# Optimization experiments

Measured on AMD Instinct MI355X. Metric: run time of the kernel, lower is better.

The kernel has to match this reference:

```python
import jax, jax.numpy as jnp
import numpy as np

B, N, D, L = 64, 512, 256, 4


def setup_inputs() -> dict:
    key = jax.random.key(0)
    ks = jax.random.split(key, 10)
    scale = 1.0 / np.sqrt(D)
    x = jax.random.normal(ks[0], (B, N, D), dtype=jnp.float32)
    adj = (jax.random.uniform(ks[1], (B, N, N)) < 0.1).astype(jnp.float32)
    return {
        "x": x,
        "adj": adj,
        "w_attn_w": jax.random.normal(ks[2], (L, D, D), dtype=jnp.float32) * scale,
        "w_attn_b": jnp.zeros((L, D), dtype=jnp.float32),
        "lin0_w": jax.random.normal(ks[3], (L, D, D), dtype=jnp.float32) * scale,
        "lin0_b": jnp.zeros((L, D), dtype=jnp.float32),
        "lin1_w": jax.random.normal(ks[4], (L, D, D), dtype=jnp.float32) * scale,
        "lin1_b": jnp.zeros((L, D), dtype=jnp.float32),
        "final_w": jax.random.normal(ks[5], (D, D), dtype=jnp.float32) * scale,
        "final_b": jnp.zeros((D,), dtype=jnp.float32),
    }


def reference(x, adj, w_attn_w, w_attn_b, lin0_w, lin0_b, lin1_w, lin1_b, final_w, final_b):
    # set self-loops on the adjacency diagonal (in-place in the torch code)
    idx = jnp.arange(N)
    adj = adj.at[:, idx, idx].set(1.0)
    eye = 1e-5 * jnp.eye(N, dtype=x.dtype)
    attls = []
    for l in range(L):
        x0 = x
        # q = w_attn[l](x): torch Linear is x @ W.T + b, W: [out,in]
        q = jnp.einsum('bnd,od->bno', x, w_attn_w[l]) + w_attn_b[l]
        adj_attn = jax.nn.sigmoid(jnp.einsum('bij,bkj->bik', q, x))  # [B,N,N]
        adj_attn = (adj_attn + eye) * adj
        adj_attn = adj_attn / jnp.sum(adj_attn, axis=-1, keepdims=True)
        attls.append(adj_attn)
        x = jnp.einsum('bij,bjd->bid', adj_attn, x)
        x = jax.nn.relu(jnp.einsum('bnd,od->bno', x, lin0_w[l]) + lin0_b[l])
        x = jax.nn.relu(jnp.einsum('bnd,od->bno', x, lin1_w[l]) + lin1_b[l])
        x = x + x0
    x = jnp.einsum('bnd,od->bno', x, final_w) + final_b
    return (x, jnp.stack(attls))
```

## Files before the change

kernel.cpp:

```cpp
#include <hip/hip_runtime.h>
#include <cstdint>

#define B_ 64
#define N_ 512
#define D_ 256
#define L_ 4

typedef __bf16 bf16;
typedef __attribute__((ext_vector_type(8))) __bf16 bf16x8;
typedef __attribute__((ext_vector_type(4))) __bf16 bf16x4;
typedef __attribute__((ext_vector_type(4))) float f32x4;

#define MFMA16(a, b, c) __builtin_amdgcn_mfma_f32_16x16x32_bf16((a), (b), (c), 0, 0, 0)

__device__ __forceinline__ float sigmoidf_(float z) {
  return 1.0f / (1.0f + __expf(-z));
}


#define BARSYNC() do { \
    asm volatile("s_waitcnt lgkmcnt(0)\n\ts_barrier" ::: "memory"); \
    __builtin_amdgcn_sched_barrier(0); \
  } while (0)

#define UIDX(u) (((size_t)(u)) * 64 + lane)

__global__ __launch_bounds__(256) void pack_w(
    const float* __restrict__ src, bf16* __restrict__ dst)
{
  const int tid = threadIdx.x, lane = tid & 63;
  const int U = blockIdx.x * 4 + (tid >> 6);
  const int m = U >> 7, u = U & 127;
  const int r16 = u >> 3, kc = u & 7;
  const int row = r16 * 16 + (lane & 15);
  const int k0 = kc * 32 + (lane >> 4) * 8;
  const float* s = src + (size_t)m * D_ * D_ + (size_t)row * D_ + k0;
  const float4 v0 = *(const float4*)s;
  const float4 v1 = *(const float4*)(s + 4);
  bf16x8 o;
  o[0] = (bf16)v0.x; o[1] = (bf16)v0.y; o[2] = (bf16)v0.z; o[3] = (bf16)v0.w;
  o[4] = (bf16)v1.x; o[5] = (bf16)v1.y; o[6] = (bf16)v1.z; o[7] = (bf16)v1.w;
  ((bf16x8*)dst)[(size_t)U * 64 + lane] = o;
}

__global__ __launch_bounds__(256) void init_pack(
    const float* __restrict__ x, bf16* __restrict__ xbpk, bf16* __restrict__ xTpk)
{
  const int tid = threadIdx.x, lane = tid & 63;
  const int U = blockIdx.x * 4 + (tid >> 6);
  const int b = U >> 9, u = U & 511;
  if (u < 256) {
    const int n = (u >> 3) * 16 + (lane & 15);
    const int d = (u & 7) * 32 + (lane >> 4) * 8;
    const float* s = x + ((size_t)(b * N_ + n)) * D_ + d;
    const float4 v0 = *(const float4*)s;
    const float4 v1 = *(const float4*)(s + 4);
    bf16x8 o;
    o[0] = (bf16)v0.x; o[1] = (bf16)v0.y; o[2] = (bf16)v0.z; o[3] = (bf16)v0.w;
    o[4] = (bf16)v1.x; o[5] = (bf16)v1.y; o[6] = (bf16)v1.z; o[7] = (bf16)v1.w;
    ((bf16x8*)xbpk)[((size_t)b * 256 + u) * 64 + lane] = o;
  } else {
    const int u2 = u - 256;
    const int d = (u2 >> 4) * 16 + (lane & 15);
    const int n = (u2 & 15) * 32 + (lane >> 4) * 8;
    bf16x8 o;
#pragma unroll
    for (int e = 0; e < 8; ++e)
      o[e] = (bf16)x[((size_t)(b * N_ + n + e)) * D_ + d];
    ((bf16x8*)xTpk)[((size_t)b * 256 + u2) * 64 + lane] = o;
  }
}

__global__ __launch_bounds__(512, 1) void gat_layer(
    const bf16* __restrict__ xbpk_in, const bf16* __restrict__ xTpk_in,
    bf16* __restrict__ xbpk_out, bf16* __restrict__ xTpk_out,
    const bf16* __restrict__ Wap, const float* __restrict__ ba,
    const bf16* __restrict__ W0p, const float* __restrict__ b0,
    const bf16* __restrict__ W1p, const float* __restrict__ b1,
    const float* __restrict__ adj, const unsigned short* __restrict__ bits_in,
    unsigned short* __restrict__ bits_out, float* __restrict__ outA)
{
  __shared__ bf16 qs[64 * 264];
  __shared__ bf16 xps[64 * 520];
  __shared__ float psum[8][64];
  __shared__ float rinvs[64];
  __shared__ unsigned int bits_s[1024];

  const int tid = threadIdx.x, w = tid >> 6, lane = tid & 63;
  const int l16 = lane & 15, quad = lane >> 4;
  const int wg = blockIdx.x;
  const int lid = (wg & 7) * 64 + (wg >> 3);
  const int b = lid >> 3;
  const int row0 = (lid & 7) * 64;

  const bf16x8* Xbp = (const bf16x8*)xbpk_in + (size_t)b * 16384;
  const bf16x8* Xtp = (const bf16x8*)xTpk_in + (size_t)b * 16384;
  bf16x8* XbpO = (bf16x8*)xbpk_out + (size_t)b * 16384;
  bf16x8* XtpO = (bf16x8*)xTpk_out + (size_t)b * 16384;
  const bf16x8* Wa8 = (const bf16x8*)Wap;
  const bf16x8* W08 = (const bf16x8*)W0p;
  const bf16x8* W18 = (const bf16x8*)W1p;

  if (bits_in) {
#pragma unroll
    for (int e = 0; e < 2; ++e) {
      const int t = tid + e * 512;
      bits_s[t] = ((const unsigned int*)bits_in)[((size_t)b * N_ + row0) * 16 + t];
    }
  }

  {
    f32x4 acc0[4][2] = {};
#pragma unroll
    for (int ks = 0; ks < 8; ++ks) {
      bf16x8 af[4];
#pragma unroll
      for (int m = 0; m < 4; ++m)
        af[m] = Xbp[UIDX(((row0 >> 4) + m) * 8 + ks)];
      bf16x8 bw[2];
#pragma unroll
      for (int i = 0; i < 2; ++i)
        bw[i] = Wa8[UIDX((2 * w + i) * 8 + ks)];
#pragma unroll
      for (int m = 0; m < 4; ++m)
#pragma unroll
        for (int i = 0; i < 2; ++i) acc0[m][i] = MFMA16(af[m], bw[i], acc0[m][i]);
    }
#pragma unroll
    for (int m = 0; m < 4; ++m)
#pragma unroll
      for (int i = 0; i < 2; ++i) {
        const int col = 32 * w + 16 * i + l16;
        const float bv = ba[col];
#pragma unroll
        for (int r = 0; r < 4; ++r)
          qs[(16 * m + quad * 4 + r) * 264 + col] = (bf16)(acc0[m][i][r] + bv);
      }
  }
  bf16x8 bxp[4][4];
#pragma unroll
  for (int ks = 0; ks < 4; ++ks)
#pragma unroll
    for (int jt = 0; jt < 4; ++jt)
      bxp[ks][jt] = Xbp[UIDX((4 * w + jt) * 8 + ks)];
  __builtin_amdgcn_sched_barrier(0);
  BARSYNC();

  float p[4][4] = {};
  bf16x8 btp[8][2];
  {
    f32x4 acc1[4][4] = {};
#pragma unroll
    for (int ks = 0; ks < 8; ++ks) {
      bf16x8 af[4];
#pragma unroll
      for (int m = 0; m < 4; ++m)
        af[m] = *(const bf16x8*)&qs[(16 * m + l16) * 264 + ks * 32 + quad * 8];
      bf16x8 bx[4];
#pragma unroll
      for (int jt = 0; jt < 4; ++jt)
        bx[jt] = (ks < 4) ? bxp[ks][jt] : Xbp[UIDX((4 * w + jt) * 8 + ks)];
#pragma unroll
      for (int m = 0; m < 4; ++m)
#pragma unroll
        for (int jt = 0; jt < 4; ++jt)
          acc1[m][jt] = MFMA16(af[m], bx[jt], acc1[m][jt]);
    }
#pragma unroll
    for (int jt = 0; jt < 4; ++jt) {
      const int lcol = 64 * w + jt * 16 + l16;
      const int piece = 4 * w + jt;
#pragma unroll
      for (int m = 0; m < 4; ++m)
#pragma unroll
        for (int r = 0; r < 4; ++r) {
          const int row = 16 * m + quad * 4 + r;
          const int grow = row0 + row;
          float av;
          if (bits_in) {
            const unsigned short m16 = ((const unsigned short*)bits_s)[row * 32 + piece];
            av = (float)((m16 >> l16) & 1);
          } else {
            av = __builtin_nontemporal_load(
                adj + ((size_t)b * N_ + grow) * N_ + lcol);
          }
          const bool diag = (grow == lcol);
          if (bits_out) {
            const unsigned long long bal = __ballot(diag || av != 0.0f);
            if (l16 == 0)
              bits_out[((size_t)b * N_ + row0 + 16 * m + 4 * quad + r) * 32 + piece] =
                  (unsigned short)((bal >> (quad * 16)) & 0xFFFFull);
          }
          const float sg = sigmoidf_(acc1[m][jt][r]);
          const float v = diag ? (sg + 1e-5f) : sg * av;
          const bf16 bv = (bf16)v;
          xps[row * 520 + lcol] = bv;
          p[m][r] += (float)bv;
        }
    }
  }
#pragma unroll
  for (int ks = 0; ks < 8; ++ks)
#pragma unroll
    for (int i = 0; i < 2; ++i)
      btp[ks][i] = Xtp[UIDX((2 * w + i) * 16 + ks)];
  __builtin_amdgcn_sched_barrier(0);

#pragma unroll
  for (int m = 0; m < 4; ++m)
#pragma unroll
    for (int r = 0; r < 4; ++r) {
#pragma unroll
      for (int msk = 1; msk < 16; msk <<= 1) p[m][r] += __shfl_xor(p[m][r], msk, 64);
    }
  if (l16 == 0) {
#pragma unroll
    for (int m = 0; m < 4; ++m)
#pragma unroll
      for (int r = 0; r < 4; ++r) psum[w][16 * m + quad * 4 + r] = p[m][r];
  }
  BARSYNC();
  if (tid < 64) {
    float s = 0.0f;
#pragma unroll
    for (int ww = 0; ww < 8; ++ww) s += psum[ww][tid];
    rinvs[tid] = 1.0f / s;
  }
  BARSYNC();

  const size_t abase = ((size_t)b * N_ + row0) * N_;
#pragma unroll
  for (int e = 0; e < 16; ++e) {
    const int idx = tid + e * 512;
    const int row = idx >> 7, c4 = (idx & 127) * 4;
    const float ri = rinvs[row];
    bf16x4 pv = *(const bf16x4*)&xps[row * 520 + c4];
    f32x4 nv;
    nv[0] = (float)pv[0] * ri; nv[1] = (float)pv[1] * ri;
    nv[2] = (float)pv[2] * ri; nv[3] = (float)pv[3] * ri;
    __builtin_nontemporal_store(nv, (f32x4*)(outA + abase + (size_t)row * N_ + c4));
    bf16x4 o;
    o[0] = (bf16)nv[0]; o[1] = (bf16)nv[1]; o[2] = (bf16)nv[2]; o[3] = (bf16)nv[3];
    *(bf16x4*)&xps[row * 520 + c4] = o;
  }
  BARSYNC();

  {
    f32x4 acc3[4][2] = {};
#pragma unroll
    for (int ks = 0; ks < 16; ++ks) {
      bf16x8 af[4];
#pragma unroll
      for (int m = 0; m < 4; ++m)
        af[m] = *(const bf16x8*)&xps[(16 * m + l16) * 520 + ks * 32 + quad * 8];
      bf16x8 bt[2];
#pragma unroll
      for (int i = 0; i < 2; ++i)
        bt[i] = (ks < 8) ? btp[ks][i] : Xtp[UIDX((2 * w + i) * 16 + ks)];
#pragma unroll
      for (int m = 0; m < 4; ++m)
#pragma unroll
        for (int i = 0; i < 2; ++i) acc3[m][i] = MFMA16(af[m], bt[i], acc3[m][i]);
    }
    bf16x8 w0r[16];
#pragma unroll
    for (int j = 0; j < 16; ++j)
      w0r[j] = W08[UIDX((2 * w + (j >> 3)) * 8 + (j & 7))];
    __builtin_amdgcn_sched_barrier(0);
#pragma unroll
    for (int m = 0; m < 4; ++m)
#pragma unroll
      for (int i = 0; i < 2; ++i) {
        const int d = 32 * w + 16 * i + l16;
#pragma unroll
        for (int r = 0; r < 4; ++r)
          qs[(16 * m + quad * 4 + r) * 264 + d] = (bf16)acc3[m][i][r];
      }
    BARSYNC();

    f32x4 acc[4][2] = {};
#pragma unroll
    for (int ks = 0; ks < 8; ++ks) {
      bf16x8 af[4];
#pragma unroll
      for (int m = 0; m < 4; ++m)
        af[m] = *(const bf16x8*)&qs[(16 * m + l16) * 264 + ks * 32 + quad * 8];
#pragma unroll
      for (int m = 0; m < 4; ++m)
#pragma unroll
        for (int i = 0; i < 2; ++i)
          acc[m][i] = MFMA16(af[m], w0r[i * 8 + ks], acc[m][i]);
    }
    bf16x8 w1r[16];
#pragma unroll
    for (int j = 0; j < 16; ++j)
      w1r[j] = W18[UIDX((2 * w + (j >> 3)) * 8 + (j & 7))];
    bf16x8 resid[4];
#pragma unroll
    for (int j = 0; j < 4; ++j) {
      const int uu = w * 4 + j;
      resid[j] = Xbp[UIDX(((row0 >> 4) + (uu >> 3)) * 8 + (uu & 7))];
    }
    __builtin_amdgcn_sched_barrier(0);
#pragma unroll
    for (int m = 0; m < 4; ++m)
#pragma unroll
      for (int i = 0; i < 2; ++i) {
        const int col = 32 * w + 16 * i + l16;
        const float bv = b0[col];
#pragma unroll
        for (int r = 0; r < 4; ++r)
          xps[(16 * m + quad * 4 + r) * 264 + col] = (bf16)fmaxf(acc[m][i][r] + bv, 0.0f);
      }
    BARSYNC();

#pragma unroll
    for (int j = 0; j < 4; ++j) {
      const int uu = w * 4 + j;
      const int rr = uu >> 3, kc = uu & 7;
      *(bf16x8*)&qs[(rr * 16 + l16) * 264 + kc * 32 + quad * 8] = resid[j];
    }
    f32x4 acc5[4][2] = {};
#pragma unroll
    for (int ks = 0; ks < 8; ++ks) {
      bf16x8 af[4];
#pragma unroll
      for (int m = 0; m < 4; ++m)
        af[m] = *(const bf16x8*)&xps[(16 * m + l16) * 264 + ks * 32 + quad * 8];
#pragma unroll
      for (int m = 0; m < 4; ++m)
#pragma unroll
        for (int i = 0; i < 2; ++i)
          acc5[m][i] = MFMA16(af[m], w1r[i * 8 + ks], acc5[m][i]);
    }
    BARSYNC();

#pragma unroll
    for (int m = 0; m < 4; ++m)
#pragma unroll
      for (int i = 0; i < 2; ++i) {
        const int d = 32 * w + 16 * i + l16;
        const float bv = b1[d];
#pragma unroll
        for (int r = 0; r < 4; ++r) {
          const int nl = 16 * m + quad * 4 + r;
          const float x0 = (float)qs[nl * 264 + d];
          const float t2 = fmaxf(acc5[m][i][r] + bv, 0.0f) + x0;
          qs[nl * 264 + d] = (bf16)t2;
        }
      }
    BARSYNC();

#pragma unroll
    for (int j = 0; j < 4; ++j) {
      const int uu = w * 4 + j;
      const int rr = uu >> 3, kc = uu & 7;
      const bf16x8 v = *(const bf16x8*)&qs[(rr * 16 + l16) * 264 + kc * 32 + quad * 8];
      XbpO[UIDX(((row0 >> 4) + rr) * 8 + kc)] = v;
    }
#pragma unroll
    for (int j = 0; j < 4; ++j) {
      const int uu = w * 4 + j;
      const int d16 = uu >> 1, nk = uu & 1;
      const int d = d16 * 16 + l16;
      bf16x8 v;
#pragma unroll
      for (int e = 0; e < 8; ++e)
        v[e] = qs[(nk * 32 + quad * 8 + e) * 264 + d];
      XtpO[UIDX(d16 * 16 + (row0 >> 5) + nk)] = v;
    }
  }
}

__global__ __launch_bounds__(256, 4) void final_proj(
    const bf16* __restrict__ xbpk, const bf16* __restrict__ Wfp,
    const float* __restrict__ bfv, float* __restrict__ outX)
{
  const int tid = threadIdx.x, w = tid >> 6, lane = tid & 63;
  const int l16 = lane & 15, quad = lane >> 4;
  const int wg = blockIdx.x;
  const int lid = (wg & 7) * 128 + (wg >> 3);
  const int row0g = lid * 32;
  const int b = row0g >> 9, n0 = row0g & 511;
  const bf16x8* Xbp = (const bf16x8*)xbpk + (size_t)b * 16384;
  const bf16x8* Wf8 = (const bf16x8*)Wfp;
  f32x4 acc[2][4] = {};
#pragma unroll
  for (int ks = 0; ks < 8; ++ks) {
    bf16x8 af[2];
#pragma unroll
    for (int m = 0; m < 2; ++m)
      af[m] = Xbp[UIDX(((n0 >> 4) + m) * 8 + ks)];
    bf16x8 bw[4];
#pragma unroll
    for (int i = 0; i < 4; ++i)
      bw[i] = Wf8[UIDX((4 * w + i) * 8 + ks)];
#pragma unroll
    for (int m = 0; m < 2; ++m)
#pragma unroll
      for (int i = 0; i < 4; ++i) acc[m][i] = MFMA16(af[m], bw[i], acc[m][i]);
  }
#pragma unroll
  for (int m = 0; m < 2; ++m)
#pragma unroll
    for (int i = 0; i < 4; ++i) {
      const int col = 64 * w + 16 * i + l16;
      const float bv = bfv[col];
#pragma unroll
      for (int r = 0; r < 4; ++r) {
        const size_t R = (size_t)row0g + 16 * m + quad * 4 + r;
        __builtin_nontemporal_store(acc[m][i][r] + bv, outX + R * D_ + col);
      }
    }
}

extern "C" void kernel_launch(void* const* d_in, const int* in_sizes, int n_in,
                              void* d_out, int out_size, void* d_ws, size_t ws_size,
                              hipStream_t stream)
{
  const float* x_in  = (const float*)d_in[0];
  const float* adj   = (const float*)d_in[1];
  const float* wattn = (const float*)d_in[2];
  const float* battn = (const float*)d_in[3];
  const float* w0    = (const float*)d_in[4];
  const float* b0    = (const float*)d_in[5];
  const float* w1    = (const float*)d_in[6];
  const float* b1    = (const float*)d_in[7];
  const float* wf    = (const float*)d_in[8];
  const float* bfin  = (const float*)d_in[9];

  float* out_x    = (float*)d_out;
  float* out_attn = out_x + (size_t)B_ * N_ * D_;

  const size_t XBN = (size_t)B_ * N_ * D_;
  const int DD2 = D_ * D_;
  bf16* wb   = (bf16*)d_ws;
  bf16* xbp0 = wb + 13 * DD2;
  bf16* xtp0 = xbp0 + XBN;
  bf16* xbp1 = xtp0 + XBN;
  bf16* xtp1 = xbp1 + XBN;
  unsigned short* bits = (unsigned short*)(xtp1 + XBN);

  pack_w<<<dim3(4 * 32), 256, 0, stream>>>(wattn, wb);
  pack_w<<<dim3(4 * 32), 256, 0, stream>>>(w0, wb + 4 * DD2);
  pack_w<<<dim3(4 * 32), 256, 0, stream>>>(w1, wb + 8 * DD2);
  pack_w<<<dim3(1 * 32), 256, 0, stream>>>(wf, wb + 12 * DD2);

  init_pack<<<dim3(8192), 256, 0, stream>>>(x_in, xbp0, xtp0);

  bf16* xbps[2] = {xbp0, xbp1};
  bf16* xtps[2] = {xtp0, xtp1};
  for (int l = 0; l < L_; ++l) {
    const int pi = l & 1, po = 1 - pi;
    gat_layer<<<dim3((N_ / 64) * B_), 512, 0, stream>>>(
        xbps[pi], xtps[pi], xbps[po], xtps[po],
        wb + l * DD2, battn + l * D_,
        wb + (4 + l) * DD2, b0 + l * D_,
        wb + (8 + l) * DD2, b1 + l * D_,
        adj, (l == 0) ? nullptr : bits, (l == 0) ? bits : nullptr,
        out_attn + (size_t)l * B_ * N_ * N_);
  }
  final_proj<<<dim3((B_ * N_) / 32), 256, 0, stream>>>(
      xbps[0], wb + 12 * DD2, bfin, out_x);
}
```

Before: 697.3 us.

## Merge weight and input packing kernels; deepen register prefetch of X tiles

Combines the four weight-packing launches and the input-packing launch into one prep kernel, indexed by block range, which removes several small launches. Inside the layer kernel, more B-operand fragments of X (6 of 8 k-steps) and of X-transpose (12 of 16) are prefetched into registers, and the loads are issued earlier so they overlap with the preceding MFMA and epilogue work. This raises register pressure and can lower occupancy or cause spills.

```diff
diff --git a/kernel.cpp b/kernel.cpp
--- a/kernel.cpp
+++ b/kernel.cpp
@@ -25,29 +25,34 @@
 
 #define UIDX(u) (((size_t)(u)) * 64 + lane)
 
-__global__ __launch_bounds__(256) void pack_w(
-    const float* __restrict__ src, bf16* __restrict__ dst)
+__global__ __launch_bounds__(256) void prep(
+    const float* __restrict__ x,
+    const float* __restrict__ wattn, const float* __restrict__ w0,
+    const float* __restrict__ w1, const float* __restrict__ wf,
+    bf16* __restrict__ wb, bf16* __restrict__ xbpk, bf16* __restrict__ xTpk)
 {
   const int tid = threadIdx.x, lane = tid & 63;
-  const int U = blockIdx.x * 4 + (tid >> 6);
-  const int m = U >> 7, u = U & 127;
-  const int r16 = u >> 3, kc = u & 7;
-  const int row = r16 * 16 + (lane & 15);
-  const int k0 = kc * 32 + (lane >> 4) * 8;
-  const float* s = src + (size_t)m * D_ * D_ + (size_t)row * D_ + k0;
-  const float4 v0 = *(const float4*)s;
-  const float4 v1 = *(const float4*)(s + 4);
-  bf16x8 o;
-  o[0] = (bf16)v0.x; o[1] = (bf16)v0.y; o[2] = (bf16)v0.z; o[3] = (bf16)v0.w;
-  o[4] = (bf16)v1.x; o[5] = (bf16)v1.y; o[6] = (bf16)v1.z; o[7] = (bf16)v1.w;
-  ((bf16x8*)dst)[(size_t)U * 64 + lane] = o;
-}
-
-__global__ __launch_bounds__(256) void init_pack(
-    const float* __restrict__ x, bf16* __restrict__ xbpk, bf16* __restrict__ xTpk)
-{
-  const int tid = threadIdx.x, lane = tid & 63;
-  const int U = blockIdx.x * 4 + (tid >> 6);
+  const int bid = blockIdx.x;
+  if (bid < 416) {
+    const int U = bid * 4 + (tid >> 6);
+    const int m = U >> 7, u = U & 127;
+    const float* src = (m < 4)  ? wattn + (size_t)m * (D_ * D_)
+                     : (m < 8)  ? w0 + (size_t)(m - 4) * (D_ * D_)
+                     : (m < 12) ? w1 + (size_t)(m - 8) * (D_ * D_)
+                                : wf;
+    const int r16 = u >> 3, kc = u & 7;
+    const int row = r16 * 16 + (lane & 15);
+    const int k0 = kc * 32 + (lane >> 4) * 8;
+    const float* s = src + (size_t)row * D_ + k0;
+    const float4 v0 = *(const float4*)s;
+    const float4 v1 = *(const float4*)(s + 4);
+    bf16x8 o;
+    o[0] = (bf16)v0.x; o[1] = (bf16)v0.y; o[2] = (bf16)v0.z; o[3] = (bf16)v0.w;
+    o[4] = (bf16)v1.x; o[5] = (bf16)v1.y; o[6] = (bf16)v1.z; o[7] = (bf16)v1.w;
+    ((bf16x8*)wb)[(size_t)U * 64 + lane] = o;
+    return;
+  }
+  const int U = (bid - 416) * 4 + (tid >> 6);
   const int b = U >> 9, u = U & 511;
   if (u < 256) {
     const int n = (u >> 3) * 16 + (lane & 15);
@@ -109,6 +114,7 @@
     }
   }
 
+  bf16x8 bxp[6][4];
   {
     f32x4 acc0[4][2] = {};
 #pragma unroll
@@ -126,6 +132,12 @@
 #pragma unroll
         for (int i = 0; i < 2; ++i) acc0[m][i] = MFMA16(af[m], bw[i], acc0[m][i]);
     }
+#pragma unroll
+    for (int ks = 0; ks < 6; ++ks)
+#pragma unroll
+      for (int jt = 0; jt < 4; ++jt)
+        bxp[ks][jt] = Xbp[UIDX((4 * w + jt) * 8 + ks)];
+    __builtin_amdgcn_sched_barrier(0);
 #pragma unroll
     for (int m = 0; m < 4; ++m)
 #pragma unroll
@@ -137,17 +149,10 @@
           qs[(16 * m + quad * 4 + r) * 264 + col] = (bf16)(acc0[m][i][r] + bv);
       }
   }
-  bf16x8 bxp[4][4];
-#pragma unroll
-  for (int ks = 0; ks < 4; ++ks)
-#pragma unroll
-    for (int jt = 0; jt < 4; ++jt)
-      bxp[ks][jt] = Xbp[UIDX((4 * w + jt) * 8 + ks)];
-  __builtin_amdgcn_sched_barrier(0);
   BARSYNC();
 
   float p[4][4] = {};
-  bf16x8 btp[8][2];
+  bf16x8 btp[12][2];
   {
     f32x4 acc1[4][4] = {};
 #pragma unroll
@@ -159,13 +164,20 @@
       bf16x8 bx[4];
 #pragma unroll
       for (int jt = 0; jt < 4; ++jt)
-        bx[jt] = (ks < 4) ? bxp[ks][jt] : Xbp[UIDX((4 * w + jt) * 8 + ks)];
+        bx[jt] = (ks < 6) ? bxp[ks][jt] : Xbp[UIDX((4 * w + jt) * 8 + ks)];
 #pragma unroll
       for (int m = 0; m < 4; ++m)
 #pragma unroll
         for (int jt = 0; jt < 4; ++jt)
           acc1[m][jt] = MFMA16(af[m], bx[jt], acc1[m][jt]);
     }
+#pragma unroll
+    for (int ks = 0; ks < 12; ++ks)
+#pragma unroll
+      for (int i = 0; i < 2; ++i)
+        btp[ks][i] = Xtp[UIDX((2 * w + i) * 16 + ks)];
+    __builtin_amdgcn_sched_barrier(0);
+
 #pragma unroll
     for (int jt = 0; jt < 4; ++jt) {
       const int lcol = 64 * w + jt * 16 + l16;
@@ -200,13 +212,6 @@
     }
   }
 #pragma unroll
-  for (int ks = 0; ks < 8; ++ks)
-#pragma unroll
-    for (int i = 0; i < 2; ++i)
-      btp[ks][i] = Xtp[UIDX((2 * w + i) * 16 + ks)];
-  __builtin_amdgcn_sched_barrier(0);
-
-#pragma unroll
   for (int m = 0; m < 4; ++m)
 #pragma unroll
     for (int r = 0; r < 4; ++r) {
@@ -256,7 +261,7 @@
       bf16x8 bt[2];
 #pragma unroll
       for (int i = 0; i < 2; ++i)
-        bt[i] = (ks < 8) ? btp[ks][i] : Xtp[UIDX((2 * w + i) * 16 + ks)];
+        bt[i] = (ks < 12) ? btp[ks][i] : Xtp[UIDX((2 * w + i) * 16 + ks)];
 #pragma unroll
       for (int m = 0; m < 4; ++m)
 #pragma unroll
@@ -441,12 +446,8 @@
   bf16* xtp1 = xbp1 + XBN;
   unsigned short* bits = (unsigned short*)(xtp1 + XBN);
 
-  pack_w<<<dim3(4 * 32), 256, 0, stream>>>(wattn, wb);
-  pack_w<<<dim3(4 * 32), 256, 0, stream>>>(w0, wb + 4 * DD2);
-  pack_w<<<dim3(4 * 32), 256, 0, stream>>>(w1, wb + 8 * DD2);
-  pack_w<<<dim3(1 * 32), 256, 0, stream>>>(wf, wb + 12 * DD2);
-
-  init_pack<<<dim3(8192), 256, 0, stream>>>(x_in, xbp0, xtp0);
+  prep<<<dim3(416 + 8192), 256, 0, stream>>>(
+      x_in, wattn, w0, w1, wf, wb, xbp0, xtp0);
 
   bf16* xbps[2] = {xbp0, xbp1};
   bf16* xtps[2] = {xtp0, xtp1};
```

Result: slower. 719.6 us (+3.2%).
